# Optimization experiments

Measured on AMD Instinct MI355X. Metric: run time of the kernel, lower is better.

Reference implementation:

```python
import jax, jax.numpy as jnp
import numpy as np

EPS = 1e-12  # torch F.normalize eps


def setup_inputs() -> dict:
    key = jax.random.key(0)
    k1, k2, k3 = jax.random.split(key, 3)
    B, D, H, W, K = 64, 512, 32, 32, 64
    x = jax.random.normal(k1, (B, D, H, W), dtype=jnp.float32)
    w = jax.random.normal(k2, (K, D), dtype=jnp.float32) * 0.05  # 1x1 conv weight
    c = jax.random.normal(k3, (K, D), dtype=jnp.float32)          # cluster centers
    return {"x": x, "w": w, "c": c}


def reference(x, w, c):
    B, D, H, W = x.shape
    K = w.shape[0]
    N = H * W
    # 1x1 conv (no bias): (B,D,H,W) x (K,D) -> (B,K,H,W)
    features = jnp.einsum('bdhw,kd->bkhw', x, w)
    # NOTE: original applies softmax over dim=2 (the H axis only)
    a_bar = jax.nn.softmax(features, axis=2)
    xf = x.reshape(B, D, N)
    a = a_bar.reshape(B, K, N)
    # V[b,k,d] = sum_n a[b,k,n] * (x[b,d,n] - c[k,d])
    V = jnp.einsum('bkn,bdn->bkd', a, xf) - a.sum(axis=2)[:, :, None] * c[None]
    V = V.transpose(2, 1, 0)  # (D, K, B)
    # F.normalize(V, p=2, dim=1) applied twice (second is idempotent)
    norm = jnp.maximum(jnp.linalg.norm(V, axis=1, keepdims=True), EPS)
    y = V / norm
    norm2 = jnp.maximum(jnp.linalg.norm(y, axis=1, keepdims=True), EPS)
    return y / norm2
```

## Files before the change

kernel.cpp:

```cpp
#include <hip/hip_runtime.h>


typedef __attribute__((ext_vector_type(8))) short short8;
typedef __attribute__((ext_vector_type(4))) float f32x4;
typedef unsigned short u16;
typedef unsigned int u32;

union S8u { u32 q[4]; short8 s; };

__device__ __forceinline__ u32 pk2(float lo, float hi) {
  union { float f; u32 u; } a, b; a.f = lo; b.f = hi;
  u32 xl = (a.u + 0x7fffu + ((a.u >> 16) & 1u)) >> 16;
  u32 xh = (b.u + 0x7fffu + ((b.u >> 16) & 1u)) & 0xffff0000u;
  return xl | xh;
}

typedef const __attribute__((address_space(1))) u32 GU32;
typedef __attribute__((address_space(3))) u32 LU32;
__device__ __forceinline__ void glds16(const void* g, void* l) {
  __builtin_amdgcn_global_load_lds((GU32*)g, (LU32*)l, 16, 0, 0);
}

__global__ __launch_bounds__(256) void k0_packw(
    const float* __restrict__ w, u16* __restrict__ wsw)
{
  const int tg = blockIdx.x * 256 + threadIdx.x;
  const int dd4 = tg & 7, i = (tg >> 3) & 15, k = tg >> 7;
  f32x4 v = *(const f32x4*)(w + k * 512 + i * 32 + dd4 * 4);
  u32* dst = (u32*)(wsw + ((size_t)i * 64 + k) * 40 + dd4 * 4);
  dst[0] = pk2(v[0], v[1]);
  dst[1] = pk2(v[2], v[3]);
}

__global__ __launch_bounds__(256, 2) void k1_features(
    const float* __restrict__ x, const u16* __restrict__ wsw,
    float* __restrict__ feat)
{
  const int blk = blockIdx.x;
  const int b = blk & 63, nt8 = blk >> 6;
  const int nb = nt8 * 128;
  const int tid = threadIdx.x, lane = tid & 63, wv = tid >> 6;
  const int row = lane & 15, q = lane >> 4;

  __shared__ __align__(16) float xs[3][32][128];
  __shared__ __align__(16) u16 wls[3][64][40];

  const char* xbase = (const char*)(x + ((size_t)b << 19) + nb);
  const char* wbase = (const char*)wsw;
  const int dd0 = tid >> 5, cby = (tid & 31) * 16;

  f32x4 acc[4][2];
#pragma unroll
  for (int mt = 0; mt < 4; mt++)
#pragma unroll
    for (int nt = 0; nt < 2; nt++) acc[mt][nt] = (f32x4){0.f, 0.f, 0.f, 0.f};

#define STAGE1(d0, buf)                                                        \
  {                                                                            \
    char* lx = (char*)&xs[buf][0][0];                                          \
    _Pragma("unroll")                                                          \
    for (int j = 0; j < 4; j++) {                                              \
      const int dd = j * 8 + dd0;                                              \
      glds16(xbase + (size_t)((d0) + dd) * 4096 + cby,                         \
             lx + j * 4096 + tid * 16);                                        \
    }                                                                          \
    char* lw = (char*)&wls[buf][0][0];                                         \
    const char* gw = wbase + (size_t)((d0) >> 5) * 5120;                       \
    glds16(gw + tid * 16, lw + tid * 16);                                      \
    if (tid < 64) glds16(gw + 4096 + tid * 16, lw + 4096 + tid * 16);          \
  }

  STAGE1(0, 0);
  STAGE1(32, 1);
  int bi = 0;
  for (int i = 0; i < 16; i++) {
    if (i == 15) asm volatile("s_waitcnt vmcnt(0)" ::: "memory");
    else         asm volatile("s_waitcnt vmcnt(5)" ::: "memory");
    __builtin_amdgcn_s_barrier();
    __builtin_amdgcn_sched_barrier(0);
    if (i < 14) {
      const int nbuf = (bi == 0) ? 2 : bi - 1;
      STAGE1((i + 2) * 32, nbuf);
    }

    short8 af[4];
#pragma unroll
    for (int mt = 0; mt < 4; mt++)
      af[mt] = *(const short8*)&wls[bi][mt * 16 + row][q * 8];
    short8 bfv[2];
#pragma unroll
    for (int nt = 0; nt < 2; nt++) {
      const int n = wv * 32 + nt * 16 + row;
      const int d8 = q * 8;
      float v0 = xs[bi][d8 + 0][n], v1 = xs[bi][d8 + 1][n];
      float v2 = xs[bi][d8 + 2][n], v3 = xs[bi][d8 + 3][n];
      float v4 = xs[bi][d8 + 4][n], v5 = xs[bi][d8 + 5][n];
      float v6 = xs[bi][d8 + 6][n], v7 = xs[bi][d8 + 7][n];
      S8u t;
      t.q[0] = pk2(v0, v1); t.q[1] = pk2(v2, v3);
      t.q[2] = pk2(v4, v5); t.q[3] = pk2(v6, v7);
      bfv[nt] = t.s;
    }
#pragma unroll
    for (int nt = 0; nt < 2; nt++)
#pragma unroll
      for (int mt = 0; mt < 4; mt++)
        acc[mt][nt] = __builtin_amdgcn_mfma_f32_16x16x32_bf16(af[mt], bfv[nt], acc[mt][nt], 0, 0, 0);

    bi = (bi == 2) ? 0 : bi + 1;
  }
#undef STAGE1

  float* fb = feat + ((size_t)b << 16);
  const int nbw = nb + wv * 32;
#pragma unroll
  for (int mt = 0; mt < 4; mt++)
#pragma unroll
    for (int nt = 0; nt < 2; nt++)
#pragma unroll
      for (int r = 0; r < 4; r++)
        fb[(mt * 16 + q * 4 + r) * 1024 + nbw + nt * 16 + row] = acc[mt][nt][r];
}

__global__ __launch_bounds__(256) void k1b_softmax(
    const float* __restrict__ feat, u16* __restrict__ apad)
{
  const int tid = threadIdx.x, wv = tid >> 6, lane = tid & 63;
  const int rid = blockIdx.x * 4 + wv;
  const int b = rid >> 6, k = rid & 63;
  const float* f = feat + ((size_t)rid << 10);
  const int wl = (lane & 7) * 4;
  const int hq = lane >> 3;

  f32x4 v[4];
#pragma unroll
  for (int r = 0; r < 4; r++)
    v[r] = *(const f32x4*)(f + (hq + r * 8) * 32 + wl);

  f32x4 m = v[0];
#pragma unroll
  for (int r = 1; r < 4; r++)
#pragma unroll
    for (int c = 0; c < 4; c++) m[c] = fmaxf(m[c], v[r][c]);
#pragma unroll
  for (int mk = 8; mk <= 32; mk <<= 1)
#pragma unroll
    for (int c = 0; c < 4; c++) m[c] = fmaxf(m[c], __shfl_xor(m[c], mk));

  f32x4 s = (f32x4){0.f, 0.f, 0.f, 0.f};
#pragma unroll
  for (int r = 0; r < 4; r++)
#pragma unroll
    for (int c = 0; c < 4; c++) { v[r][c] = __expf(v[r][c] - m[c]); s[c] += v[r][c]; }
#pragma unroll
  for (int mk = 8; mk <= 32; mk <<= 1)
#pragma unroll
    for (int c = 0; c < 4; c++) s[c] += __shfl_xor(s[c], mk);

  f32x4 inv;
#pragma unroll
  for (int c = 0; c < 4; c++) inv[c] = 1.0f / s[c];

#pragma unroll
  for (int r = 0; r < 4; r++) {
    const int h = hq + r * 8;
    u32* dst = (u32*)(apad + ((size_t)(b * 32 + h) * 64 + k) * 40 + wl);
    dst[0] = pk2(v[r][0] * inv[0], v[r][1] * inv[1]);
    dst[1] = pk2(v[r][2] * inv[2], v[r][3] * inv[3]);
  }
}

__global__ __launch_bounds__(256, 2) void k2_aggregate(
    const float* __restrict__ x, const u16* __restrict__ apad,
    const float* __restrict__ cc, float* __restrict__ yw)
{
  const int blk = blockIdx.x;
  const int b = blk & 63, dt = blk >> 6;
  const int tid = threadIdx.x, lane = tid & 63, wv = tid >> 6;
  const int row = lane & 15, q = lane >> 4;

  __shared__ __align__(16) u16 als[3][64][40];

  const char* abase = (const char*)(apad + (size_t)b * 32 * 64 * 40);
  const float* px0 = x + ((size_t)b << 19) + (size_t)(dt * 64 + wv * 16 + row) * 1024 + q * 8;

#define STAGEA(i, buf)                                                         \
  {                                                                            \
    char* la = (char*)&als[buf][0][0];                                         \
    const char* ga = abase + (size_t)(i) * 5120;                               \
    glds16(ga + tid * 16, la + tid * 16);                                      \
    if (tid < 64) glds16(ga + 4096 + tid * 16, la + 4096 + tid * 16);          \
  }

  f32x4 acc[4];
#pragma unroll
  for (int mt = 0; mt < 4; mt++) acc[mt] = (f32x4){0.f, 0.f, 0.f, 0.f};

  STAGEA(0, 0);
  f32x4 c0 = *(const f32x4*)px0;
  f32x4 c1 = *(const f32x4*)(px0 + 4);
  STAGEA(1, 1);
  int bi = 0;
  for (int i = 0; i < 32; i++) {
    if (i == 31) asm volatile("s_waitcnt vmcnt(0)" ::: "memory");
    else         asm volatile("s_waitcnt vmcnt(3)" ::: "memory");
    __builtin_amdgcn_s_barrier();
    __builtin_amdgcn_sched_barrier(0);
    f32x4 p0, p1;
    if (i < 31) {
      p0 = *(const f32x4*)(px0 + (i + 1) * 32);
      p1 = *(const f32x4*)(px0 + (i + 1) * 32 + 4);
    }
    if (i < 30) {
      const int nbuf = (bi == 0) ? 2 : bi - 1;
      STAGEA(i + 2, nbuf);
    }
    S8u t;
    t.q[0] = pk2(c0[0], c0[1]); t.q[1] = pk2(c0[2], c0[3]);
    t.q[2] = pk2(c1[0], c1[1]); t.q[3] = pk2(c1[2], c1[3]);
    const short8 bfv = t.s;
#pragma unroll
    for (int mt = 0; mt < 4; mt++) {
      short8 af = *(const short8*)&als[bi][mt * 16 + row][q * 8];
      acc[mt] = __builtin_amdgcn_mfma_f32_16x16x32_bf16(af, bfv, acc[mt], 0, 0, 0);
    }
    c0 = p0; c1 = p1;
    bi = (bi == 2) ? 0 : bi + 1;
  }
#undef STAGEA

  const int dcol = dt * 64 + wv * 16 + row;
  float v[16]; float ss = 0.f;
#pragma unroll
  for (int mt = 0; mt < 4; mt++)
#pragma unroll
    for (int r = 0; r < 4; r++) {
      const int k = mt * 16 + q * 4 + r;
      const float tv = acc[mt][r] - 32.0f * cc[k * 512 + dcol];
      v[mt * 4 + r] = tv; ss += tv * tv;
    }
  ss += __shfl_xor(ss, 16);
  ss += __shfl_xor(ss, 32);
  const float rn = 1.0f / fmaxf(sqrtf(ss), 1e-12f);
  float* yb = yw + ((size_t)b << 15) + dcol;
#pragma unroll
  for (int mt = 0; mt < 4; mt++)
#pragma unroll
    for (int r = 0; r < 4; r++)
      yb[(size_t)(mt * 16 + q * 4 + r) << 9] = v[mt * 4 + r] * rn;
}

__global__ __launch_bounds__(256) void k3_transpose(
    const float* __restrict__ yw, float* __restrict__ out)
{
  const int blk = blockIdx.x;
  const int k = blk & 63;
  const int dt = blk >> 6;
  const int d0 = dt * 64;
  const int tid = threadIdx.x;
  __shared__ float T[64][68];
  {
    const int bl = tid >> 2, seg = tid & 3;
    const float* src = yw + (size_t)bl * 32768 + k * 512 + d0 + seg * 16;
#pragma unroll
    for (int i = 0; i < 4; i++) {
      f32x4 v = *(const f32x4*)(src + i * 4);
#pragma unroll
      for (int jj = 0; jj < 4; jj++) T[seg * 16 + i * 4 + jj][bl] = v[jj];
    }
  }
  __syncthreads();
  {
    const int dl = tid >> 2, bseg = tid & 3;
    float* dst = out + (size_t)(d0 + dl) * 4096 + k * 64 + bseg * 16;
    const float* srcT = &T[dl][bseg * 16];
#pragma unroll
    for (int i = 0; i < 4; i++)
      *(f32x4*)(dst + i * 4) = *(const f32x4*)(srcT + i * 4);
  }
}

extern "C" void kernel_launch(void* const* d_in, const int* in_sizes, int n_in,
                              void* d_out, int out_size, void* d_ws, size_t ws_size,
                              hipStream_t stream) {
  const float* x = (const float*)d_in[0];
  const float* w = (const float*)d_in[1];
  const float* c = (const float*)d_in[2];
  float* out = (float*)d_out;
  char* ws = (char*)d_ws;
  float* feat = (float*)ws;
  u16*   apad = (u16*)(ws + (size_t)16 * 1024 * 1024);
  float* yw   = (float*)(ws + (size_t)26 * 1024 * 1024);
  u16*   wsw  = (u16*)(ws + (size_t)34 * 1024 * 1024);
  k0_packw    <<<dim3(32),   dim3(256), 0, stream>>>(w, wsw);
  k1_features <<<dim3(512),  dim3(256), 0, stream>>>(x, wsw, feat);
  k1b_softmax <<<dim3(1024), dim3(256), 0, stream>>>(feat, apad);
  k2_aggregate<<<dim3(512),  dim3(256), 0, stream>>>(x, apad, c, yw);
  k3_transpose<<<dim3(512),  dim3(256), 0, stream>>>(yw, out);
}
```

Measured before the change: 235.1 us.

## Load MFMA A-operands from global into registers and split feature tiles finer

The packed weight and softmax-weight buffers drop their padded stride of 40 for a dense stride of 32. Both GEMM kernels now read the A operand (weights or softmax weights) straight from global memory into registers, with software prefetch several steps ahead, instead of staging it through LDS. The feature kernel's N tile is halved to 64 with a 4-deep x pipeline and runs twice as many blocks at occupancy hint 3. The aggregate kernel drops LDS and barriers entirely, prefetching x four iterations ahead. This removes LDS traffic and barrier stalls, at the cost of more register pressure and more redundant global or L2 reads of the shared weights.

```diff
diff --git a/kernel.cpp b/kernel.cpp
--- a/kernel.cpp
+++ b/kernel.cpp
@@ -27,99 +27,90 @@
   const int tg = blockIdx.x * 256 + threadIdx.x;
   const int dd4 = tg & 7, i = (tg >> 3) & 15, k = tg >> 7;
   f32x4 v = *(const f32x4*)(w + k * 512 + i * 32 + dd4 * 4);
-  u32* dst = (u32*)(wsw + ((size_t)i * 64 + k) * 40 + dd4 * 4);
+  u32* dst = (u32*)(wsw + (size_t)(i * 64 + k) * 32 + dd4 * 4);
   dst[0] = pk2(v[0], v[1]);
   dst[1] = pk2(v[2], v[3]);
 }
 
-__global__ __launch_bounds__(256, 2) void k1_features(
+__global__ __launch_bounds__(256, 3) void k1_features(
     const float* __restrict__ x, const u16* __restrict__ wsw,
     float* __restrict__ feat)
 {
   const int blk = blockIdx.x;
-  const int b = blk & 63, nt8 = blk >> 6;
-  const int nb = nt8 * 128;
+  const int b = blk & 63, nt = blk >> 6;
+  const int nb = nt * 64;
   const int tid = threadIdx.x, lane = tid & 63, wv = tid >> 6;
   const int row = lane & 15, q = lane >> 4;
 
-  __shared__ __align__(16) float xs[3][32][128];
-  __shared__ __align__(16) u16 wls[3][64][40];
+  __shared__ __align__(16) float xs[4][32][64];
 
   const char* xbase = (const char*)(x + ((size_t)b << 19) + nb);
-  const char* wbase = (const char*)wsw;
-  const int dd0 = tid >> 5, cby = (tid & 31) * 16;
-
-  f32x4 acc[4][2];
-#pragma unroll
-  for (int mt = 0; mt < 4; mt++)
-#pragma unroll
-    for (int nt = 0; nt < 2; nt++) acc[mt][nt] = (f32x4){0.f, 0.f, 0.f, 0.f};
-
-#define STAGE1(d0, buf)                                                        \
+  const int r0 = tid >> 4, cb = (tid & 15) * 16;
+
+  f32x4 acc[4];
+#pragma unroll
+  for (int mt = 0; mt < 4; mt++) acc[mt] = (f32x4){0.f, 0.f, 0.f, 0.f};
+
+  short8 wf[4][4];
+
+#define STAGE1(s)                                                              \
   {                                                                            \
-    char* lx = (char*)&xs[buf][0][0];                                          \
+    char* lx = (char*)&xs[(s) & 3][0][0];                                      \
+    const char* gx = xbase + (size_t)(s) * 131072;                             \
+    glds16(gx + (size_t)r0 * 4096 + cb, lx + r0 * 256 + cb);                   \
+    glds16(gx + (size_t)(r0 + 16) * 4096 + cb, lx + (r0 + 16) * 256 + cb);     \
+  }
+#define LOADW(s)                                                               \
+  {                                                                            \
     _Pragma("unroll")                                                          \
-    for (int j = 0; j < 4; j++) {                                              \
-      const int dd = j * 8 + dd0;                                              \
-      glds16(xbase + (size_t)((d0) + dd) * 4096 + cby,                         \
-             lx + j * 4096 + tid * 16);                                        \
-    }                                                                          \
-    char* lw = (char*)&wls[buf][0][0];                                         \
-    const char* gw = wbase + (size_t)((d0) >> 5) * 5120;                       \
-    glds16(gw + tid * 16, lw + tid * 16);                                      \
-    if (tid < 64) glds16(gw + 4096 + tid * 16, lw + 4096 + tid * 16);          \
-  }
-
-  STAGE1(0, 0);
-  STAGE1(32, 1);
-  int bi = 0;
+    for (int mt = 0; mt < 4; mt++)                                             \
+      wf[(s) & 3][mt] = *(const short8*)(                                      \
+          wsw + (size_t)(((s) * 64 + mt * 16 + row) * 32 + q * 8));            \
+  }
+
+  STAGE1(0); __builtin_amdgcn_sched_barrier(0);
+  LOADW(0);  __builtin_amdgcn_sched_barrier(0);
+  STAGE1(1); __builtin_amdgcn_sched_barrier(0);
+  LOADW(1);  __builtin_amdgcn_sched_barrier(0);
+  STAGE1(2); __builtin_amdgcn_sched_barrier(0);
+  LOADW(2);  __builtin_amdgcn_sched_barrier(0);
+
+#pragma unroll
   for (int i = 0; i < 16; i++) {
-    if (i == 15) asm volatile("s_waitcnt vmcnt(0)" ::: "memory");
-    else         asm volatile("s_waitcnt vmcnt(5)" ::: "memory");
+    if (i == 14)      asm volatile("s_waitcnt vmcnt(10)" ::: "memory");
+    else if (i == 15) asm volatile("s_waitcnt vmcnt(4)" ::: "memory");
+    else              asm volatile("s_waitcnt vmcnt(16)" ::: "memory");
     __builtin_amdgcn_s_barrier();
     __builtin_amdgcn_sched_barrier(0);
-    if (i < 14) {
-      const int nbuf = (bi == 0) ? 2 : bi - 1;
-      STAGE1((i + 2) * 32, nbuf);
-    }
-
-    short8 af[4];
+    if (i < 13) {
+      STAGE1(i + 3); __builtin_amdgcn_sched_barrier(0);
+      LOADW(i + 3);  __builtin_amdgcn_sched_barrier(0);
+    }
+
+    const float* xr = &xs[i & 3][0][wv * 16 + row];
+    const int d8 = q * 8;
+    float v0 = xr[(d8 + 0) * 64], v1 = xr[(d8 + 1) * 64];
+    float v2 = xr[(d8 + 2) * 64], v3 = xr[(d8 + 3) * 64];
+    float v4 = xr[(d8 + 4) * 64], v5 = xr[(d8 + 5) * 64];
+    float v6 = xr[(d8 + 6) * 64], v7 = xr[(d8 + 7) * 64];
+    S8u t;
+    t.q[0] = pk2(v0, v1); t.q[1] = pk2(v2, v3);
+    t.q[2] = pk2(v4, v5); t.q[3] = pk2(v6, v7);
+    const short8 bfv = t.s;
 #pragma unroll
     for (int mt = 0; mt < 4; mt++)
-      af[mt] = *(const short8*)&wls[bi][mt * 16 + row][q * 8];
-    short8 bfv[2];
-#pragma unroll
-    for (int nt = 0; nt < 2; nt++) {
-      const int n = wv * 32 + nt * 16 + row;
-      const int d8 = q * 8;
-      float v0 = xs[bi][d8 + 0][n], v1 = xs[bi][d8 + 1][n];
-      float v2 = xs[bi][d8 + 2][n], v3 = xs[bi][d8 + 3][n];
-      float v4 = xs[bi][d8 + 4][n], v5 = xs[bi][d8 + 5][n];
-      float v6 = xs[bi][d8 + 6][n], v7 = xs[bi][d8 + 7][n];
-      S8u t;
-      t.q[0] = pk2(v0, v1); t.q[1] = pk2(v2, v3);
-      t.q[2] = pk2(v4, v5); t.q[3] = pk2(v6, v7);
-      bfv[nt] = t.s;
-    }
-#pragma unroll
-    for (int nt = 0; nt < 2; nt++)
-#pragma unroll
-      for (int mt = 0; mt < 4; mt++)
-        acc[mt][nt] = __builtin_amdgcn_mfma_f32_16x16x32_bf16(af[mt], bfv[nt], acc[mt][nt], 0, 0, 0);
-
-    bi = (bi == 2) ? 0 : bi + 1;
+      acc[mt] = __builtin_amdgcn_mfma_f32_16x16x32_bf16(wf[i & 3][mt], bfv, acc[mt], 0, 0, 0);
   }
 #undef STAGE1
+#undef LOADW
 
   float* fb = feat + ((size_t)b << 16);
-  const int nbw = nb + wv * 32;
+  const int nbw = nb + wv * 16 + row;
 #pragma unroll
   for (int mt = 0; mt < 4; mt++)
 #pragma unroll
-    for (int nt = 0; nt < 2; nt++)
-#pragma unroll
-      for (int r = 0; r < 4; r++)
-        fb[(mt * 16 + q * 4 + r) * 1024 + nbw + nt * 16 + row] = acc[mt][nt][r];
+    for (int r = 0; r < 4; r++)
+      fb[(mt * 16 + q * 4 + r) * 1024 + nbw] = acc[mt][r];
 }
 
 __global__ __launch_bounds__(256) void k1b_softmax(
@@ -164,7 +155,7 @@
 #pragma unroll
   for (int r = 0; r < 4; r++) {
     const int h = hq + r * 8;
-    u32* dst = (u32*)(apad + ((size_t)(b * 32 + h) * 64 + k) * 40 + wl);
+    u32* dst = (u32*)(apad + ((size_t)(b * 32 + h) * 64 + k) * 32 + wl);
     dst[0] = pk2(v[r][0] * inv[0], v[r][1] * inv[1]);
     dst[1] = pk2(v[r][2] * inv[2], v[r][3] * inv[3]);
   }
@@ -179,55 +170,46 @@
   const int tid = threadIdx.x, lane = tid & 63, wv = tid >> 6;
   const int row = lane & 15, q = lane >> 4;
 
-  __shared__ __align__(16) u16 als[3][64][40];
-
-  const char* abase = (const char*)(apad + (size_t)b * 32 * 64 * 40);
   const float* px0 = x + ((size_t)b << 19) + (size_t)(dt * 64 + wv * 16 + row) * 1024 + q * 8;
-
-#define STAGEA(i, buf)                                                         \
-  {                                                                            \
-    char* la = (char*)&als[buf][0][0];                                         \
-    const char* ga = abase + (size_t)(i) * 5120;                               \
-    glds16(ga + tid * 16, la + tid * 16);                                      \
-    if (tid < 64) glds16(ga + 4096 + tid * 16, la + 4096 + tid * 16);          \
-  }
+  const u16* ab = apad + ((size_t)b << 16) + (size_t)row * 32 + q * 8;
 
   f32x4 acc[4];
 #pragma unroll
   for (int mt = 0; mt < 4; mt++) acc[mt] = (f32x4){0.f, 0.f, 0.f, 0.f};
 
-  STAGEA(0, 0);
-  f32x4 c0 = *(const f32x4*)px0;
-  f32x4 c1 = *(const f32x4*)(px0 + 4);
-  STAGEA(1, 1);
-  int bi = 0;
+  f32x4 xp0[4], xp1[4];
+  short8 ap[3][4];
+#pragma unroll
+  for (int j = 0; j < 4; j++) {
+    xp0[j] = *(const f32x4*)(px0 + j * 32);
+    xp1[j] = *(const f32x4*)(px0 + j * 32 + 4);
+  }
+#pragma unroll
+  for (int j = 0; j < 2; j++)
+#pragma unroll
+    for (int mt = 0; mt < 4; mt++)
+      ap[j][mt] = *(const short8*)(ab + (size_t)j * 2048 + mt * 512);
+
+#pragma unroll
   for (int i = 0; i < 32; i++) {
-    if (i == 31) asm volatile("s_waitcnt vmcnt(0)" ::: "memory");
-    else         asm volatile("s_waitcnt vmcnt(3)" ::: "memory");
-    __builtin_amdgcn_s_barrier();
-    __builtin_amdgcn_sched_barrier(0);
-    f32x4 p0, p1;
-    if (i < 31) {
-      p0 = *(const f32x4*)(px0 + (i + 1) * 32);
-      p1 = *(const f32x4*)(px0 + (i + 1) * 32 + 4);
-    }
-    if (i < 30) {
-      const int nbuf = (bi == 0) ? 2 : bi - 1;
-      STAGEA(i + 2, nbuf);
-    }
+    const f32x4 c0 = xp0[i & 3], c1 = xp1[i & 3];
     S8u t;
     t.q[0] = pk2(c0[0], c0[1]); t.q[1] = pk2(c0[2], c0[3]);
     t.q[2] = pk2(c1[0], c1[1]); t.q[3] = pk2(c1[2], c1[3]);
     const short8 bfv = t.s;
 #pragma unroll
-    for (int mt = 0; mt < 4; mt++) {
-      short8 af = *(const short8*)&als[bi][mt * 16 + row][q * 8];
-      acc[mt] = __builtin_amdgcn_mfma_f32_16x16x32_bf16(af, bfv, acc[mt], 0, 0, 0);
-    }
-    c0 = p0; c1 = p1;
-    bi = (bi == 2) ? 0 : bi + 1;
-  }
-#undef STAGEA
+    for (int mt = 0; mt < 4; mt++)
+      acc[mt] = __builtin_amdgcn_mfma_f32_16x16x32_bf16(ap[i % 3][mt], bfv, acc[mt], 0, 0, 0);
+    if (i + 4 < 32) {
+      xp0[i & 3] = *(const f32x4*)(px0 + (i + 4) * 32);
+      xp1[i & 3] = *(const f32x4*)(px0 + (i + 4) * 32 + 4);
+    }
+    if (i + 2 < 32) {
+#pragma unroll
+      for (int mt = 0; mt < 4; mt++)
+        ap[(i + 2) % 3][mt] = *(const short8*)(ab + (size_t)(i + 2) * 2048 + mt * 512);
+    }
+  }
 
   const int dcol = dt * 64 + wv * 16 + row;
   float v[16]; float ss = 0.f;
@@ -293,7 +275,7 @@
   float* yw   = (float*)(ws + (size_t)26 * 1024 * 1024);
   u16*   wsw  = (u16*)(ws + (size_t)34 * 1024 * 1024);
   k0_packw    <<<dim3(32),   dim3(256), 0, stream>>>(w, wsw);
-  k1_features <<<dim3(512),  dim3(256), 0, stream>>>(x, wsw, feat);
+  k1_features <<<dim3(1024), dim3(256), 0, stream>>>(x, wsw, feat);
   k1b_softmax <<<dim3(1024), dim3(256), 0, stream>>>(feat, apad);
   k2_aggregate<<<dim3(512),  dim3(256), 0, stream>>>(x, apad, c, yw);
   k3_transpose<<<dim3(512),  dim3(256), 0, stream>>>(yw, out);
```

Result: slower. 242.8 us (+3.3%).

## Switch GEMM kernels to double buffering and halve aggregate block size

Applied to the files above, without the earlier changes.

Replaces the triple-buffered pipelines in the feature and aggregate kernels with double buffering synchronised by plain __syncthreads. This frees LDS and simplifies the manual vmcnt waits. The aggregate kernel now runs 1024 blocks of 128 threads, each covering 32 D columns instead of 64, to raise parallelism and occupancy. The trade-off is a shallower prefetch, because __syncthreads waits for all outstanding loads, so global latency may be hidden less well.

```diff
diff --git a/kernel.cpp b/kernel.cpp
--- a/kernel.cpp
+++ b/kernel.cpp
@@ -42,8 +42,8 @@
   const int tid = threadIdx.x, lane = tid & 63, wv = tid >> 6;
   const int row = lane & 15, q = lane >> 4;
 
-  __shared__ __align__(16) float xs[3][32][128];
-  __shared__ __align__(16) u16 wls[3][64][40];
+  __shared__ __align__(16) float xs[2][32][128];
+  __shared__ __align__(16) u16 wls[2][64][40];
 
   const char* xbase = (const char*)(x + ((size_t)b << 19) + nb);
   const char* wbase = (const char*)wsw;
@@ -71,31 +71,24 @@
   }
 
   STAGE1(0, 0);
-  STAGE1(32, 1);
-  int bi = 0;
   for (int i = 0; i < 16; i++) {
-    if (i == 15) asm volatile("s_waitcnt vmcnt(0)" ::: "memory");
-    else         asm volatile("s_waitcnt vmcnt(5)" ::: "memory");
-    __builtin_amdgcn_s_barrier();
-    __builtin_amdgcn_sched_barrier(0);
-    if (i < 14) {
-      const int nbuf = (bi == 0) ? 2 : bi - 1;
-      STAGE1((i + 2) * 32, nbuf);
-    }
+    const int buf = i & 1;
+    __syncthreads();
+    if (i < 15) STAGE1((i + 1) * 32, buf ^ 1);
 
     short8 af[4];
 #pragma unroll
     for (int mt = 0; mt < 4; mt++)
-      af[mt] = *(const short8*)&wls[bi][mt * 16 + row][q * 8];
+      af[mt] = *(const short8*)&wls[buf][mt * 16 + row][q * 8];
     short8 bfv[2];
 #pragma unroll
     for (int nt = 0; nt < 2; nt++) {
       const int n = wv * 32 + nt * 16 + row;
       const int d8 = q * 8;
-      float v0 = xs[bi][d8 + 0][n], v1 = xs[bi][d8 + 1][n];
-      float v2 = xs[bi][d8 + 2][n], v3 = xs[bi][d8 + 3][n];
-      float v4 = xs[bi][d8 + 4][n], v5 = xs[bi][d8 + 5][n];
-      float v6 = xs[bi][d8 + 6][n], v7 = xs[bi][d8 + 7][n];
+      float v0 = xs[buf][d8 + 0][n], v1 = xs[buf][d8 + 1][n];
+      float v2 = xs[buf][d8 + 2][n], v3 = xs[buf][d8 + 3][n];
+      float v4 = xs[buf][d8 + 4][n], v5 = xs[buf][d8 + 5][n];
+      float v6 = xs[buf][d8 + 6][n], v7 = xs[buf][d8 + 7][n];
       S8u t;
       t.q[0] = pk2(v0, v1); t.q[1] = pk2(v2, v3);
       t.q[2] = pk2(v4, v5); t.q[3] = pk2(v6, v7);
@@ -106,8 +99,6 @@
 #pragma unroll
       for (int mt = 0; mt < 4; mt++)
         acc[mt][nt] = __builtin_amdgcn_mfma_f32_16x16x32_bf16(af[mt], bfv[nt], acc[mt][nt], 0, 0, 0);
-
-    bi = (bi == 2) ? 0 : bi + 1;
   }
 #undef STAGE1
 
@@ -170,7 +161,7 @@
   }
 }
 
-__global__ __launch_bounds__(256, 2) void k2_aggregate(
+__global__ __launch_bounds__(128, 2) void k2_aggregate(
     const float* __restrict__ x, const u16* __restrict__ apad,
     const float* __restrict__ cc, float* __restrict__ yw)
 {
@@ -179,16 +170,17 @@
   const int tid = threadIdx.x, lane = tid & 63, wv = tid >> 6;
   const int row = lane & 15, q = lane >> 4;
 
-  __shared__ __align__(16) u16 als[3][64][40];
+  __shared__ __align__(16) u16 als[2][64][40];
 
   const char* abase = (const char*)(apad + (size_t)b * 32 * 64 * 40);
-  const float* px0 = x + ((size_t)b << 19) + (size_t)(dt * 64 + wv * 16 + row) * 1024 + q * 8;
+  const float* px0 = x + ((size_t)b << 19) + (size_t)(dt * 32 + wv * 16 + row) * 1024 + q * 8;
 
 #define STAGEA(i, buf)                                                         \
   {                                                                            \
     char* la = (char*)&als[buf][0][0];                                         \
     const char* ga = abase + (size_t)(i) * 5120;                               \
     glds16(ga + tid * 16, la + tid * 16);                                      \
+    glds16(ga + 2048 + tid * 16, la + 2048 + tid * 16);                        \
     if (tid < 64) glds16(ga + 4096 + tid * 16, la + 4096 + tid * 16);          \
   }
 
@@ -199,21 +191,14 @@
   STAGEA(0, 0);
   f32x4 c0 = *(const f32x4*)px0;
   f32x4 c1 = *(const f32x4*)(px0 + 4);
-  STAGEA(1, 1);
-  int bi = 0;
+  f32x4 p0, p1;
   for (int i = 0; i < 32; i++) {
-    if (i == 31) asm volatile("s_waitcnt vmcnt(0)" ::: "memory");
-    else         asm volatile("s_waitcnt vmcnt(3)" ::: "memory");
-    __builtin_amdgcn_s_barrier();
-    __builtin_amdgcn_sched_barrier(0);
-    f32x4 p0, p1;
+    const int buf = i & 1;
+    __syncthreads();
     if (i < 31) {
+      STAGEA(i + 1, buf ^ 1);
       p0 = *(const f32x4*)(px0 + (i + 1) * 32);
       p1 = *(const f32x4*)(px0 + (i + 1) * 32 + 4);
-    }
-    if (i < 30) {
-      const int nbuf = (bi == 0) ? 2 : bi - 1;
-      STAGEA(i + 2, nbuf);
     }
     S8u t;
     t.q[0] = pk2(c0[0], c0[1]); t.q[1] = pk2(c0[2], c0[3]);
@@ -221,15 +206,14 @@
     const short8 bfv = t.s;
 #pragma unroll
     for (int mt = 0; mt < 4; mt++) {
-      short8 af = *(const short8*)&als[bi][mt * 16 + row][q * 8];
+      short8 af = *(const short8*)&als[buf][mt * 16 + row][q * 8];
       acc[mt] = __builtin_amdgcn_mfma_f32_16x16x32_bf16(af, bfv, acc[mt], 0, 0, 0);
     }
     c0 = p0; c1 = p1;
-    bi = (bi == 2) ? 0 : bi + 1;
   }
 #undef STAGEA
 
-  const int dcol = dt * 64 + wv * 16 + row;
+  const int dcol = dt * 32 + wv * 16 + row;
   float v[16]; float ss = 0.f;
 #pragma unroll
   for (int mt = 0; mt < 4; mt++)
@@ -295,6 +279,6 @@
   k0_packw    <<<dim3(32),   dim3(256), 0, stream>>>(w, wsw);
   k1_features <<<dim3(512),  dim3(256), 0, stream>>>(x, wsw, feat);
   k1b_softmax <<<dim3(1024), dim3(256), 0, stream>>>(feat, apad);
-  k2_aggregate<<<dim3(512),  dim3(256), 0, stream>>>(x, apad, c, yw);
+  k2_aggregate<<<dim3(1024), dim3(128), 0, stream>>>(x, apad, c, yw);
   k3_transpose<<<dim3(512),  dim3(256), 0, stream>>>(yw, out);
 }
```

After: 230.7 us. No clear change (-1.9%).
